# Optimization experiments

Hardware: AMD Instinct MI355X
Metric: run time of the kernel (lower is better)

The kernel has to match this reference:

```python
import math
import jax, jax.numpy as jnp
import numpy as np

N, S, D = 1024, 256, 256
C, R, CLASSES = 256, 64, 1000


def setup_inputs() -> dict:
    key = jax.random.key(0)
    ks = jax.random.split(key, 10)
    inv_sqrt_d = 1.0 / math.sqrt(D)
    return {
        "q": jax.random.normal(ks[0], (N, D), dtype=jnp.float32),
        "K": jax.random.normal(ks[1], (N, S, D), dtype=jnp.float32),
        "V": jax.random.normal(ks[2], (N, S, D), dtype=jnp.float32),
        "codebook": jax.random.normal(ks[3], (C, D), dtype=jnp.float32) * inv_sqrt_d,
        "residual_codebook": jax.random.normal(ks[4], (R, D), dtype=jnp.float32) * inv_sqrt_d,
        "Wq": jax.random.normal(ks[5], (D, D), dtype=jnp.float32) * inv_sqrt_d,
        "residual_logit": jnp.zeros((), dtype=jnp.float32),
        "Wc": jax.random.normal(ks[6], (CLASSES, D), dtype=jnp.float32) * inv_sqrt_d,
        "bc": jnp.zeros((CLASSES,), dtype=jnp.float32),
        "Wr": jax.random.normal(ks[7], (D, D), dtype=jnp.float32) * inv_sqrt_d,
        "br": jnp.zeros((D,), dtype=jnp.float32),
    }


def reference(q, K, V, codebook, residual_codebook, Wq, residual_logit, Wc, bc, Wr, br):
    scale = math.sqrt(q.shape[-1])
    q_proj = q @ Wq.T  # [N,D]

    # --- base codebook pass ---
    code_weights = jax.nn.softmax(jnp.einsum('nd,cd->nc', q_proj, codebook) / scale, axis=-1)
    slot_code_weights = jax.nn.softmax(jnp.einsum('nsd,cd->nsc', K, codebook) / scale, axis=-1)
    slot_code_summaries = jnp.einsum('nsc,nsd->ncd', slot_code_weights, V)
    base_summary = jnp.einsum('nc,ncd->nd', code_weights, slot_code_summaries)
    base_weights = jnp.einsum('nc,nsc->ns', code_weights, slot_code_weights)

    # --- residual quantization pass ---
    query_residual = q_proj - code_weights @ codebook
    slot_residual = K - jnp.einsum('nsc,cd->nsd', slot_code_weights, codebook)
    residual_code_weights = jax.nn.softmax(
        jnp.einsum('nd,rd->nr', query_residual, residual_codebook) / scale, axis=-1)
    residual_slot_code_weights = jax.nn.softmax(
        jnp.einsum('nsd,rd->nsr', slot_residual, residual_codebook) / scale, axis=-1)
    residual_slot_summaries = jnp.einsum('nsr,nsd->nrd', residual_slot_code_weights, V)
    residual_summary = jnp.einsum('nr,nrd->nd', residual_code_weights, residual_slot_summaries)
    residual_weights = jnp.einsum('nr,nsr->ns', residual_code_weights, residual_slot_code_weights)

    gate = jax.nn.sigmoid(residual_logit)
    summary = base_summary + gate * residual_summary
    effective_weights = (base_weights + gate * residual_weights) / (1.0 + gate)

    logits = summary @ Wc.T + bc
    recon = summary @ Wr.T + br
    return (logits, recon, effective_weights)
```

## Files before the change

### kernel.cpp

```cpp
#include <hip/hip_runtime.h>
#include <hip/hip_bf16.h>
#include <math.h>

#define N_   1024
#define S_   256
#define D_   256
#define C_   256
#define R_   64
#define CLS_ 1000
#define INV16 0.0625f

typedef unsigned short ushortT;
typedef unsigned int uint32;
typedef short bf8 __attribute__((ext_vector_type(8)));
typedef float f4 __attribute__((ext_vector_type(4)));

static __device__ __forceinline__ float bf2f(uint32 u){
  return __uint_as_float(u << 16);
}
static __device__ __forceinline__ ushortT f2bf(float f){
  uint32 x = __float_as_uint(f);
  uint32 r = x + 0x7FFFu + ((x >> 16) & 1u);
  return (ushortT)(r >> 16);
}
static __device__ __forceinline__ uint32 packbf(float a, float b){
  return ((uint32)f2bf(b) << 16) | (uint32)f2bf(a);
}
static __device__ __forceinline__ float wred_max(float v){
  for (int o = 32; o; o >>= 1) v = fmaxf(v, __shfl_xor(v, o));
  return v;
}
static __device__ __forceinline__ float wred_sum(float v){
  for (int o = 32; o; o >>= 1) v += __shfl_xor(v, o);
  return v;
}
static __device__ __forceinline__ int swz(int row, int colbyte){
  return row*512 + ((colbyte & ~15) ^ ((row & 7) << 4)) + (colbyte & 15);
}
static __device__ __forceinline__ int pkidx(int row, int col, int nfrag){
  int ks = col >> 5, hi = (col >> 3) & 3, e = col & 7;
  int frag = row >> 4, l15p = row & 15;
  return ((ks*nfrag + frag)*64 + hi*16 + l15p)*8 + e;
}

__global__ __launch_bounds__(256) void k0(const float* __restrict__ cb,
    const float* __restrict__ rcb, const float* __restrict__ Wc,
    const float* __restrict__ Wr, ushortT* __restrict__ a1pk,
    ushortT* __restrict__ Wcr_bf, float* __restrict__ MT_f32,
    ushortT* __restrict__ mtpk)
{
  __shared__ float rl[D_];
  int bid = blockIdx.x, t = threadIdx.x;
  int gtid = bid*256 + t;
  int stride = gridDim.x*256;
  for (int e = gtid; e < (C_ + R_)*D_; e += stride){
    int row = e >> 8, col = e & 255;
    float v = (row < C_) ? cb[e] : rcb[e - C_*D_];
    a1pk[pkidx(row, col, 20)] = f2bf(v);
  }
  for (int e = gtid; e < CLS_*D_; e += stride) Wcr_bf[e] = f2bf(Wc[e]);
  for (int e = gtid; e < D_*D_; e += stride)  Wcr_bf[CLS_*D_ + e] = f2bf(Wr[e]);
  for (int e = gtid; e < 24*D_; e += stride)  Wcr_bf[1256*D_ + e] = 0;

  if (bid < R_){
    rl[t] = rcb[bid*D_ + t];
    __syncthreads();
    float acc = 0.f;
    const float* crow = cb + t*D_;
    #pragma unroll 8
    for (int k = 0; k < D_; k += 4){
      float4 w = *(const float4*)(crow + k);
      acc += w.x*rl[k] + w.y*rl[k+1] + w.z*rl[k+2] + w.w*rl[k+3];
    }
    MT_f32[bid*C_ + t] = acc;
    mtpk[pkidx(bid, t, 4)] = f2bf(acc);
  }
}

#define G4 4
__global__ __launch_bounds__(256) void k1(const float* __restrict__ q,
    const float* __restrict__ cb, const float* __restrict__ rcb,
    const float* __restrict__ Wq, const float* __restrict__ MT_f32,
    float* __restrict__ cw_ws, float* __restrict__ rcw_ws)
{
  __shared__ float qv[G4][D_], qp[G4][D_], cwl[G4][C_];
  __shared__ float redA[G4][4], redB2[G4][4];
  int n0 = blockIdx.x*G4, t = threadIdx.x;
  #pragma unroll
  for (int g = 0; g < G4; g++) qv[g][t] = q[(n0+g)*D_ + t];
  __syncthreads();
  {
    float acc[G4] = {0.f,0.f,0.f,0.f};
    const float* wrow = Wq + t*D_;
    #pragma unroll 4
    for (int k = 0; k < D_; k += 4){
      float4 w = *(const float4*)(wrow + k);
      #pragma unroll
      for (int g = 0; g < G4; g++)
        acc[g] += qv[g][k]*w.x + qv[g][k+1]*w.y + qv[g][k+2]*w.z + qv[g][k+3]*w.w;
    }
    #pragma unroll
    for (int g = 0; g < G4; g++) qp[g][t] = acc[g];
  }
  __syncthreads();
  float L[G4] = {0.f,0.f,0.f,0.f};
  {
    const float* crow = cb + t*D_;
    #pragma unroll 4
    for (int k = 0; k < D_; k += 4){
      float4 w = *(const float4*)(crow + k);
      #pragma unroll
      for (int g = 0; g < G4; g++)
        L[g] += qp[g][k]*w.x + qp[g][k+1]*w.y + qp[g][k+2]*w.z + qp[g][k+3]*w.w;
    }
  }
  float m[G4], e[G4], s[G4];
  #pragma unroll
  for (int g = 0; g < G4; g++){ L[g] *= INV16; m[g] = wred_max(L[g]); }
  if ((t & 63) == 0)
    #pragma unroll
    for (int g = 0; g < G4; g++) redA[g][t >> 6] = m[g];
  __syncthreads();
  #pragma unroll
  for (int g = 0; g < G4; g++){
    m[g] = fmaxf(fmaxf(redA[g][0], redA[g][1]), fmaxf(redA[g][2], redA[g][3]));
    e[g] = __expf(L[g] - m[g]);
    s[g] = wred_sum(e[g]);
  }
  if ((t & 63) == 0)
    #pragma unroll
    for (int g = 0; g < G4; g++) redB2[g][t >> 6] = s[g];
  __syncthreads();
  #pragma unroll
  for (int g = 0; g < G4; g++){
    float ss = redB2[g][0] + redB2[g][1] + redB2[g][2] + redB2[g][3];
    float w = e[g] / ss;
    cwl[g][t] = w;
    cw_ws[(n0+g)*C_ + t] = w;
  }
  __syncthreads();
  if (t < R_){
    float qd[G4] = {0.f,0.f,0.f,0.f}, md[G4] = {0.f,0.f,0.f,0.f};
    const float* rrow = rcb + t*D_;
    const float* mrow = MT_f32 + t*C_;
    #pragma unroll 4
    for (int k = 0; k < D_; k += 4){
      float4 wv = *(const float4*)(rrow + k);
      float4 mv = *(const float4*)(mrow + k);
      #pragma unroll
      for (int g = 0; g < G4; g++){
        qd[g] += qp[g][k]*wv.x + qp[g][k+1]*wv.y + qp[g][k+2]*wv.z + qp[g][k+3]*wv.w;
        md[g] += cwl[g][k]*mv.x + cwl[g][k+1]*mv.y + cwl[g][k+2]*mv.z + cwl[g][k+3]*mv.w;
      }
    }
    #pragma unroll
    for (int g = 0; g < G4; g++){
      float Lr = (qd[g] - md[g]) * INV16;
      float mr = wred_max(Lr);
      float er = __expf(Lr - mr);
      float sr = wred_sum(er);
      rcw_ws[(n0+g)*R_ + t] = er / sr;
    }
  }
}

__global__ __launch_bounds__(256) void k2a(const float* __restrict__ Kt,
    const ushortT* __restrict__ a1pk, const ushortT* __restrict__ mtpk,
    const float* __restrict__ cw_ws, const float* __restrict__ rcw_ws,
    const float* __restrict__ rlogit, float* __restrict__ comb_ws,
    float* __restrict__ out_ew)
{
  __shared__ __align__(16) ushortT Ktile[64*256];
  __shared__ __align__(16) ushortT Wtile[64*256];
  __shared__ float redS[4][64], redW[4][64];

  int bx  = blockIdx.x;
  int n   = bx >> 2;
  int s0  = (bx & 3) * 64;
  int tid = threadIdx.x;
  int lane = tid & 63, w = tid >> 6;
  int l15 = lane & 15, l4 = lane >> 4;
  float gate  = 1.f / (1.f + __expf(-rlogit[0]));
  float inv1g = 1.f / (1.f + gate);

  const float* Kn = Kt + (size_t)n*S_*D_ + (size_t)s0*D_;

  #pragma unroll
  for (int j = 0; j < 8; j++){
    int ch = tid + j*256;
    int row = ch >> 5, blk = ch & 31;
    const float* src = Kn + row*D_ + blk*8;
    float4 a = *(const float4*)src;
    float4 b = *(const float4*)(src + 4);
    uint4 wv = {packbf(a.x,a.y), packbf(a.z,a.w), packbf(b.x,b.y), packbf(b.z,b.w)};
    *(uint4*)((char*)Ktile + swz(row, blk*16)) = wv;
  }
  __syncthreads();

  const ushortT* a1b = a1pk + (size_t)lane*8;
  bf8 bnxC[4], bnxR[4];
  #pragma unroll
  for (int f = 0; f < 4; f++){
    bnxC[f] = *(const bf8*)(a1b + (size_t)((w + 4*f)*64)*8);
    bnxR[f] = *(const bf8*)(a1b + (size_t)((16 + f)*64)*8);
  }
  f4 accC[4][4]; f4 accR[4];
  #pragma unroll
  for (int f = 0; f < 4; f++){
    accR[f] = (f4)0.f;
    #pragma unroll
    for (int sj = 0; sj < 4; sj++) accC[f][sj] = (f4)0.f;
  }
  #pragma unroll
  for (int ks = 0; ks < 8; ks++){
    bf8 kf0 = *(const bf8*)((const char*)Ktile + swz(     l15, ks*64 + l4*16));
    bf8 kf1 = *(const bf8*)((const char*)Ktile + swz(16 + l15, ks*64 + l4*16));
    bf8 kf2 = *(const bf8*)((const char*)Ktile + swz(32 + l15, ks*64 + l4*16));
    bf8 kf3 = *(const bf8*)((const char*)Ktile + swz(48 + l15, ks*64 + l4*16));
    bf8 kfw = *(const bf8*)((const char*)Ktile + swz(w*16 + l15, ks*64 + l4*16));
    #pragma unroll
    for (int f = 0; f < 4; f++){
      bf8 aC = bnxC[f], aR = bnxR[f];
      if (ks < 7){
        bnxC[f] = *(const bf8*)(a1b + (size_t)(((ks+1)*20 + w + 4*f)*64)*8);
        bnxR[f] = *(const bf8*)(a1b + (size_t)(((ks+1)*20 + 16 + f)*64)*8);
      }
      accC[f][0] = __builtin_amdgcn_mfma_f32_16x16x32_bf16(aC, kf0, accC[f][0], 0, 0, 0);
      accC[f][1] = __builtin_amdgcn_mfma_f32_16x16x32_bf16(aC, kf1, accC[f][1], 0, 0, 0);
      accC[f][2] = __builtin_amdgcn_mfma_f32_16x16x32_bf16(aC, kf2, accC[f][2], 0, 0, 0);
      accC[f][3] = __builtin_amdgcn_mfma_f32_16x16x32_bf16(aC, kf3, accC[f][3], 0, 0, 0);
      accR[f]    = __builtin_amdgcn_mfma_f32_16x16x32_bf16(aR, kfw, accR[f],    0, 0, 0);
    }
  }

  float4 cwv[4];
  #pragma unroll
  for (int f = 0; f < 4; f++)
    cwv[f] = *(const float4*)(cw_ws + n*C_ + (w + 4*f)*16 + l4*4);
  float se[4] = {0,0,0,0}, sb[4] = {0,0,0,0};
  #pragma unroll
  for (int f = 0; f < 4; f++){
    int cbyte = ((w + 4*f)*16 + l4*4) * 2;
    #pragma unroll
    for (int sj = 0; sj < 4; sj++){
      float e0 = __expf(accC[f][sj][0] * INV16);
      float e1 = __expf(accC[f][sj][1] * INV16);
      float e2 = __expf(accC[f][sj][2] * INV16);
      float e3 = __expf(accC[f][sj][3] * INV16);
      se[sj] += (e0 + e1) + (e2 + e3);
      sb[sj] += e0*cwv[f].x + e1*cwv[f].y + e2*cwv[f].z + e3*cwv[f].w;
      int s_ = sj*16 + l15;
      *(uint32*)((char*)Wtile + swz(s_, cbyte))     = packbf(e0, e1);
      *(uint32*)((char*)Wtile + swz(s_, cbyte + 4)) = packbf(e2, e3);
    }
  }
  #pragma unroll
  for (int sj = 0; sj < 4; sj++){
    se[sj] += __shfl_xor(se[sj], 16); se[sj] += __shfl_xor(se[sj], 32);
    sb[sj] += __shfl_xor(sb[sj], 16); sb[sj] += __shfl_xor(sb[sj], 32);
  }
  if (l4 == 0){
    #pragma unroll
    for (int sj = 0; sj < 4; sj++){
      redS[w][sj*16 + l15] = se[sj];
      redW[w][sj*16 + l15] = sb[sj];
    }
  }
  __syncthreads();

  float bw_q, rcp_q;
  {
    int sq = w*16 + l15;
    float sS = redS[0][sq] + redS[1][sq] + redS[2][sq] + redS[3][sq];
    float sW = redW[0][sq] + redW[1][sq] + redW[2][sq] + redW[3][sq];
    bw_q  = sW / sS;
    rcp_q = 1.f / sS;
  }

  const ushortT* mtb = mtpk + (size_t)lane*8;
  bf8 mnx[4];
  #pragma unroll
  for (int fr = 0; fr < 4; fr++)
    mnx[fr] = *(const bf8*)(mtb + (size_t)(fr*64)*8);
  f4 wm[4];
  #pragma unroll
  for (int fr = 0; fr < 4; fr++) wm[fr] = (f4)0.f;
  #pragma unroll
  for (int ks = 0; ks < 8; ks++){
    bf8 wb = *(const bf8*)((const char*)Wtile + swz(w*16 + l15, ks*64 + l4*16));
    #pragma unroll
    for (int fr = 0; fr < 4; fr++){
      bf8 a = mnx[fr];
      if (ks < 7) mnx[fr] = *(const bf8*)(mtb + (size_t)(((ks+1)*4 + fr)*64)*8);
      wm[fr] = __builtin_amdgcn_mfma_f32_16x16x32_bf16(a, wb, wm[fr], 0, 0, 0);
    }
  }

  float4 rcwv = *(const float4*)(rcw_ws + n*R_ + 0);
  float se3 = 0.f, sc3 = 0.f;
  #pragma unroll
  for (int fr = 0; fr < 4; fr++){
    float4 rv = *(const float4*)(rcw_ws + n*R_ + fr*16 + l4*4);
    float e0 = __expf((accR[fr][0] - wm[fr][0]*rcp_q) * INV16);
    float e1 = __expf((accR[fr][1] - wm[fr][1]*rcp_q) * INV16);
    float e2 = __expf((accR[fr][2] - wm[fr][2]*rcp_q) * INV16);
    float e3 = __expf((accR[fr][3] - wm[fr][3]*rcp_q) * INV16);
    se3 += (e0 + e1) + (e2 + e3);
    sc3 += e0*rv.x + e1*rv.y + e2*rv.z + e3*rv.w;
  }
  (void)rcwv;
  se3 += __shfl_xor(se3, 16); se3 += __shfl_xor(se3, 32);
  sc3 += __shfl_xor(sc3, 16); sc3 += __shfl_xor(sc3, 32);
  float comb = bw_q + gate * (sc3 / se3);
  if (l4 == 0){
    int sabs = n*S_ + s0 + w*16 + l15;
    out_ew[sabs]  = comb * inv1g;
    comb_ws[sabs] = comb;
  }
}

__global__ __launch_bounds__(256) void k2b(const float* __restrict__ Vt,
    const float* __restrict__ comb_ws, float* __restrict__ sum_ws)
{
  __shared__ float cl[S_];
  __shared__ float4 part[4][64];
  int n = blockIdx.x, tid = threadIdx.x;
  int lane = tid & 63, w = tid >> 6;
  cl[tid] = comb_ws[n*S_ + tid];
  __syncthreads();
  const float* Vn = Vt + (size_t)n*S_*D_ + (size_t)(w*64)*D_ + lane*4;
  float4 a0 = {0,0,0,0}, a1 = {0,0,0,0};
  #pragma unroll 8
  for (int j = 0; j < 64; j += 2){
    float4 v0 = *(const float4*)(Vn + (size_t)j*D_);
    float4 v1 = *(const float4*)(Vn + (size_t)(j+1)*D_);
    float c0 = cl[w*64 + j], c1 = cl[w*64 + j + 1];
    a0.x = fmaf(c0, v0.x, a0.x); a0.y = fmaf(c0, v0.y, a0.y);
    a0.z = fmaf(c0, v0.z, a0.z); a0.w = fmaf(c0, v0.w, a0.w);
    a1.x = fmaf(c1, v1.x, a1.x); a1.y = fmaf(c1, v1.y, a1.y);
    a1.z = fmaf(c1, v1.z, a1.z); a1.w = fmaf(c1, v1.w, a1.w);
  }
  float4 acc = {a0.x+a1.x, a0.y+a1.y, a0.z+a1.z, a0.w+a1.w};
  part[w][lane] = acc;
  __syncthreads();
  if (tid < 64){
    float4 p0 = part[0][tid], p1 = part[1][tid], p2 = part[2][tid], p3 = part[3][tid];
    float4 r = {p0.x+p1.x+p2.x+p3.x, p0.y+p1.y+p2.y+p3.y,
                p0.z+p1.z+p2.z+p3.z, p0.w+p1.w+p2.w+p3.w};
    *(float4*)(sum_ws + (size_t)n*D_ + tid*4) = r;
  }
}

__global__ __launch_bounds__(256) void k3(const float* __restrict__ sum_ws,
    const ushortT* __restrict__ Wcr_bf, const float* __restrict__ bc,
    const float* __restrict__ br, float* __restrict__ out)
{
  __shared__ __align__(16) ushortT Stile[64*256];
  int bx = blockIdx.x;
  int ot = bx >> 4;
  int nt = bx & 15;
  int tid = threadIdx.x;
  int lane = tid & 63, wid = tid >> 6;
  int l15 = lane & 15, l4 = lane >> 4;

  const float* Sp = sum_ws + (size_t)nt*64*D_;
  #pragma unroll
  for (int j = 0; j < 8; j++){
    int ch = tid + j*256;
    int row = ch >> 5, blk = ch & 31;
    const float* src = Sp + row*D_ + blk*8;
    float4 a = *(const float4*)src;
    float4 b = *(const float4*)(src + 4);
    uint4 wv = {packbf(a.x,a.y), packbf(a.z,a.w), packbf(b.x,b.y), packbf(b.z,b.w)};
    *(uint4*)((char*)Stile + swz(row, blk*16)) = wv;
  }
  __syncthreads();

  int o0 = ot*64 + wid*16;
  const ushortT* Ap = Wcr_bf + (size_t)(o0 + l15)*D_ + l4*8;
  f4 acc[4];
  #pragma unroll
  for (int j = 0; j < 4; j++) acc[j] = (f4)0.f;
  #pragma unroll
  for (int k = 0; k < 8; k++){
    bf8 a = *(const bf8*)(Ap + k*32);
    #pragma unroll
    for (int nj = 0; nj < 4; nj++){
      bf8 b = *(const bf8*)((const char*)Stile + swz(nj*16 + l15, k*64 + l4*16));
      acc[nj] = __builtin_amdgcn_mfma_f32_16x16x32_bf16(a, b, acc[nj], 0, 0, 0);
    }
  }
  int obase = o0 + l4*4;
  if (obase < 1256){
    float4 bias;
    if (obase < CLS_) bias = *(const float4*)(bc + obase);
    else              bias = *(const float4*)(br + (obase - CLS_));
    #pragma unroll
    for (int nj = 0; nj < 4; nj++){
      int nn = nt*64 + nj*16 + l15;
      float4 v = {acc[nj][0]+bias.x, acc[nj][1]+bias.y, acc[nj][2]+bias.z, acc[nj][3]+bias.w};
      if (obase < CLS_) *(float4*)(out + (size_t)nn*CLS_ + obase) = v;
      else              *(float4*)(out + (size_t)N_*CLS_ + (size_t)nn*D_ + (obase - CLS_)) = v;
    }
  }
}

extern "C" void kernel_launch(void* const* d_in, const int* in_sizes, int n_in,
                              void* d_out, int out_size, void* d_ws, size_t ws_size,
                              hipStream_t stream)
{
  const float* q    = (const float*)d_in[0];
  const float* Kt   = (const float*)d_in[1];
  const float* Vt   = (const float*)d_in[2];
  const float* cb   = (const float*)d_in[3];
  const float* rcb  = (const float*)d_in[4];
  const float* Wq   = (const float*)d_in[5];
  const float* rlg  = (const float*)d_in[6];
  const float* Wc   = (const float*)d_in[7];
  const float* bc   = (const float*)d_in[8];
  const float* Wr   = (const float*)d_in[9];
  const float* br   = (const float*)d_in[10];
  float* out = (float*)d_out;
  float* ws  = (float*)d_ws;

  float* cw_ws   = ws;
  float* rcw_ws  = ws + 262144;
  float* sum_ws  = ws + 327680;
  float* comb_ws = ws + 589824;
  float* MT_f32  = ws + 851968;
  ushortT* a1pk   = (ushortT*)(ws + 868352);
  ushortT* mtpk   = a1pk + (C_ + R_)*D_;
  ushortT* Wcr_bf = mtpk + R_*C_;

  float* out_logits = out;
  float* out_ew     = out + (size_t)N_*CLS_ + (size_t)N_*D_;

  k0 <<<128,   256, 0, stream>>>(cb, rcb, Wc, Wr, a1pk, Wcr_bf, MT_f32, mtpk);
  k1 <<<N_/G4, 256, 0, stream>>>(q, cb, rcb, Wq, MT_f32, cw_ws, rcw_ws);
  k2a<<<N_*4,  256, 0, stream>>>(Kt, a1pk, mtpk, cw_ws, rcw_ws, rlg, comb_ws, out_ew);
  k2b<<<N_,    256, 0, stream>>>(Vt, comb_ws, sum_ws);
  k3 <<<320,   256, 0, stream>>>(sum_ws, Wcr_bf, bc, br, out_logits);
}
```

Baseline: 232.0 us.

## Halve k2a slot tile to 32 and split residual work across warp pairs

The k2a kernel now handles 32 slots per block instead of 64 and launches twice as many blocks, with a launch-bounds hint asking for four blocks per CU. The residual-codebook MFMAs are split so warp pairs share R fragments across the two 16-slot groups, and an extra shared-memory reduction combines their partial softmax sums. The aim is lower register and LDS use per block for higher occupancy, and better latency hiding on the memory-bound K stream. In exchange, the shared codebook fragments are reloaded by twice as many blocks, and each block pays an additional barrier.

```diff
diff --git a/kernel.cpp b/kernel.cpp
--- a/kernel.cpp
+++ b/kernel.cpp
@@ -164,29 +164,32 @@
   }
 }
 
-__global__ __launch_bounds__(256) void k2a(const float* __restrict__ Kt,
+__global__ __launch_bounds__(256, 4) void k2a(const float* __restrict__ Kt,
     const ushortT* __restrict__ a1pk, const ushortT* __restrict__ mtpk,
     const float* __restrict__ cw_ws, const float* __restrict__ rcw_ws,
     const float* __restrict__ rlogit, float* __restrict__ comb_ws,
     float* __restrict__ out_ew)
 {
-  __shared__ __align__(16) ushortT Ktile[64*256];
-  __shared__ __align__(16) ushortT Wtile[64*256];
-  __shared__ float redS[4][64], redW[4][64];
+  __shared__ __align__(16) ushortT Ktile[32*256];
+  __shared__ __align__(16) ushortT Wtile[32*256];
+  __shared__ float redS[4][32], redW[4][32];
+  __shared__ float red3S[4][32], red3W[4][32];
 
   int bx  = blockIdx.x;
-  int n   = bx >> 2;
-  int s0  = (bx & 3) * 64;
+  int n   = bx >> 3;
+  int s0  = (bx & 7) * 32;
   int tid = threadIdx.x;
   int lane = tid & 63, w = tid >> 6;
   int l15 = lane & 15, l4 = lane >> 4;
+  int rp  = w >> 1;
+  int sjr = w & 1;
   float gate  = 1.f / (1.f + __expf(-rlogit[0]));
   float inv1g = 1.f / (1.f + gate);
 
   const float* Kn = Kt + (size_t)n*S_*D_ + (size_t)s0*D_;
 
   #pragma unroll
-  for (int j = 0; j < 8; j++){
+  for (int j = 0; j < 4; j++){
     int ch = tid + j*256;
     int row = ch >> 5, blk = ch & 31;
     const float* src = Kn + row*D_ + blk*8;
@@ -198,51 +201,55 @@
   __syncthreads();
 
   const ushortT* a1b = a1pk + (size_t)lane*8;
-  bf8 bnxC[4], bnxR[4];
-  #pragma unroll
-  for (int f = 0; f < 4; f++){
+  bf8 bnxC[4], bnxR[2];
+  #pragma unroll
+  for (int f = 0; f < 4; f++)
     bnxC[f] = *(const bf8*)(a1b + (size_t)((w + 4*f)*64)*8);
-    bnxR[f] = *(const bf8*)(a1b + (size_t)((16 + f)*64)*8);
-  }
-  f4 accC[4][4]; f4 accR[4];
-  #pragma unroll
-  for (int f = 0; f < 4; f++){
-    accR[f] = (f4)0.f;
-    #pragma unroll
-    for (int sj = 0; sj < 4; sj++) accC[f][sj] = (f4)0.f;
-  }
+  #pragma unroll
+  for (int i = 0; i < 2; i++)
+    bnxR[i] = *(const bf8*)(a1b + (size_t)((16 + 2*rp + i)*64)*8);
+  f4 accC[4][2]; f4 accR[2];
+  accR[0] = (f4)0.f; accR[1] = (f4)0.f;
+  #pragma unroll
+  for (int f = 0; f < 4; f++){ accC[f][0] = (f4)0.f; accC[f][1] = (f4)0.f; }
   #pragma unroll
   for (int ks = 0; ks < 8; ks++){
     bf8 kf0 = *(const bf8*)((const char*)Ktile + swz(     l15, ks*64 + l4*16));
     bf8 kf1 = *(const bf8*)((const char*)Ktile + swz(16 + l15, ks*64 + l4*16));
-    bf8 kf2 = *(const bf8*)((const char*)Ktile + swz(32 + l15, ks*64 + l4*16));
-    bf8 kf3 = *(const bf8*)((const char*)Ktile + swz(48 + l15, ks*64 + l4*16));
-    bf8 kfw = *(const bf8*)((const char*)Ktile + swz(w*16 + l15, ks*64 + l4*16));
+    bf8 kfr = sjr ? kf1 : kf0;
     #pragma unroll
     for (int f = 0; f < 4; f++){
-      bf8 aC = bnxC[f], aR = bnxR[f];
-      if (ks < 7){
+      bf8 aC = bnxC[f];
+      if (ks < 7)
         bnxC[f] = *(const bf8*)(a1b + (size_t)(((ks+1)*20 + w + 4*f)*64)*8);
-        bnxR[f] = *(const bf8*)(a1b + (size_t)(((ks+1)*20 + 16 + f)*64)*8);
-      }
       accC[f][0] = __builtin_amdgcn_mfma_f32_16x16x32_bf16(aC, kf0, accC[f][0], 0, 0, 0);
       accC[f][1] = __builtin_amdgcn_mfma_f32_16x16x32_bf16(aC, kf1, accC[f][1], 0, 0, 0);
-      accC[f][2] = __builtin_amdgcn_mfma_f32_16x16x32_bf16(aC, kf2, accC[f][2], 0, 0, 0);
-      accC[f][3] = __builtin_amdgcn_mfma_f32_16x16x32_bf16(aC, kf3, accC[f][3], 0, 0, 0);
-      accR[f]    = __builtin_amdgcn_mfma_f32_16x16x32_bf16(aR, kfw, accR[f],    0, 0, 0);
-    }
-  }
+    }
+    #pragma unroll
+    for (int i = 0; i < 2; i++){
+      bf8 aR = bnxR[i];
+      if (ks < 7)
+        bnxR[i] = *(const bf8*)(a1b + (size_t)(((ks+1)*20 + 16 + 2*rp + i)*64)*8);
+      accR[i] = __builtin_amdgcn_mfma_f32_16x16x32_bf16(aR, kfr, accR[i], 0, 0, 0);
+    }
+  }
+
+  const ushortT* mtb = mtpk + (size_t)lane*8;
+  bf8 mnx[2];
+  #pragma unroll
+  for (int i = 0; i < 2; i++)
+    mnx[i] = *(const bf8*)(mtb + (size_t)((2*rp + i)*64)*8);
 
   float4 cwv[4];
   #pragma unroll
   for (int f = 0; f < 4; f++)
     cwv[f] = *(const float4*)(cw_ws + n*C_ + (w + 4*f)*16 + l4*4);
-  float se[4] = {0,0,0,0}, sb[4] = {0,0,0,0};
+  float se[2] = {0,0}, sb[2] = {0,0};
   #pragma unroll
   for (int f = 0; f < 4; f++){
     int cbyte = ((w + 4*f)*16 + l4*4) * 2;
     #pragma unroll
-    for (int sj = 0; sj < 4; sj++){
+    for (int sj = 0; sj < 2; sj++){
       float e0 = __expf(accC[f][sj][0] * INV16);
       float e1 = __expf(accC[f][sj][1] * INV16);
       float e2 = __expf(accC[f][sj][2] * INV16);
@@ -255,13 +262,13 @@
     }
   }
   #pragma unroll
-  for (int sj = 0; sj < 4; sj++){
+  for (int sj = 0; sj < 2; sj++){
     se[sj] += __shfl_xor(se[sj], 16); se[sj] += __shfl_xor(se[sj], 32);
     sb[sj] += __shfl_xor(sb[sj], 16); sb[sj] += __shfl_xor(sb[sj], 32);
   }
   if (l4 == 0){
     #pragma unroll
-    for (int sj = 0; sj < 4; sj++){
+    for (int sj = 0; sj < 2; sj++){
       redS[w][sj*16 + l15] = se[sj];
       redW[w][sj*16 + l15] = sb[sj];
     }
@@ -270,52 +277,55 @@
 
   float bw_q, rcp_q;
   {
-    int sq = w*16 + l15;
+    int sq = sjr*16 + l15;
     float sS = redS[0][sq] + redS[1][sq] + redS[2][sq] + redS[3][sq];
     float sW = redW[0][sq] + redW[1][sq] + redW[2][sq] + redW[3][sq];
-    bw_q  = sW / sS;
     rcp_q = 1.f / sS;
-  }
-
-  const ushortT* mtb = mtpk + (size_t)lane*8;
-  bf8 mnx[4];
-  #pragma unroll
-  for (int fr = 0; fr < 4; fr++)
-    mnx[fr] = *(const bf8*)(mtb + (size_t)(fr*64)*8);
-  f4 wm[4];
-  #pragma unroll
-  for (int fr = 0; fr < 4; fr++) wm[fr] = (f4)0.f;
+    bw_q  = sW * rcp_q;
+  }
+
+  f4 wm[2]; wm[0] = (f4)0.f; wm[1] = (f4)0.f;
   #pragma unroll
   for (int ks = 0; ks < 8; ks++){
-    bf8 wb = *(const bf8*)((const char*)Wtile + swz(w*16 + l15, ks*64 + l4*16));
-    #pragma unroll
-    for (int fr = 0; fr < 4; fr++){
-      bf8 a = mnx[fr];
-      if (ks < 7) mnx[fr] = *(const bf8*)(mtb + (size_t)(((ks+1)*4 + fr)*64)*8);
-      wm[fr] = __builtin_amdgcn_mfma_f32_16x16x32_bf16(a, wb, wm[fr], 0, 0, 0);
-    }
-  }
-
-  float4 rcwv = *(const float4*)(rcw_ws + n*R_ + 0);
+    bf8 wb = *(const bf8*)((const char*)Wtile + swz(sjr*16 + l15, ks*64 + l4*16));
+    #pragma unroll
+    for (int i = 0; i < 2; i++){
+      bf8 a = mnx[i];
+      if (ks < 7)
+        mnx[i] = *(const bf8*)(mtb + (size_t)(((ks+1)*4 + 2*rp + i)*64)*8);
+      wm[i] = __builtin_amdgcn_mfma_f32_16x16x32_bf16(a, wb, wm[i], 0, 0, 0);
+    }
+  }
+
   float se3 = 0.f, sc3 = 0.f;
   #pragma unroll
-  for (int fr = 0; fr < 4; fr++){
-    float4 rv = *(const float4*)(rcw_ws + n*R_ + fr*16 + l4*4);
-    float e0 = __expf((accR[fr][0] - wm[fr][0]*rcp_q) * INV16);
-    float e1 = __expf((accR[fr][1] - wm[fr][1]*rcp_q) * INV16);
-    float e2 = __expf((accR[fr][2] - wm[fr][2]*rcp_q) * INV16);
-    float e3 = __expf((accR[fr][3] - wm[fr][3]*rcp_q) * INV16);
+  for (int i = 0; i < 2; i++){
+    float4 rv = *(const float4*)(rcw_ws + n*R_ + (2*rp + i)*16 + l4*4);
+    float e0 = __expf((accR[i][0] - wm[i][0]*rcp_q) * INV16);
+    float e1 = __expf((accR[i][1] - wm[i][1]*rcp_q) * INV16);
+    float e2 = __expf((accR[i][2] - wm[i][2]*rcp_q) * INV16);
+    float e3 = __expf((accR[i][3] - wm[i][3]*rcp_q) * INV16);
     se3 += (e0 + e1) + (e2 + e3);
     sc3 += e0*rv.x + e1*rv.y + e2*rv.z + e3*rv.w;
   }
-  (void)rcwv;
   se3 += __shfl_xor(se3, 16); se3 += __shfl_xor(se3, 32);
   sc3 += __shfl_xor(sc3, 16); sc3 += __shfl_xor(sc3, 32);
-  float comb = bw_q + gate * (sc3 / se3);
   if (l4 == 0){
-    int sabs = n*S_ + s0 + w*16 + l15;
-    out_ew[sabs]  = comb * inv1g;
-    comb_ws[sabs] = comb;
+    red3S[w][sjr*16 + l15] = se3;
+    red3W[w][sjr*16 + l15] = sc3;
+  }
+  __syncthreads();
+
+  if (w < 2){
+    int sq = w*16 + l15;
+    float sS3 = red3S[w][sq] + red3S[w + 2][sq];
+    float sW3 = red3W[w][sq] + red3W[w + 2][sq];
+    float comb = bw_q + gate * (sW3 / sS3);
+    if (l4 == 0){
+      int sabs = n*S_ + s0 + sq;
+      out_ew[sabs]  = comb * inv1g;
+      comb_ws[sabs] = comb;
+    }
   }
 }
 
@@ -437,7 +447,7 @@
 
   k0 <<<128,   256, 0, stream>>>(cb, rcb, Wc, Wr, a1pk, Wcr_bf, MT_f32, mtpk);
   k1 <<<N_/G4, 256, 0, stream>>>(q, cb, rcb, Wq, MT_f32, cw_ws, rcw_ws);
-  k2a<<<N_*4,  256, 0, stream>>>(Kt, a1pk, mtpk, cw_ws, rcw_ws, rlg, comb_ws, out_ew);
+  k2a<<<N_*8,  256, 0, stream>>>(Kt, a1pk, mtpk, cw_ws, rcw_ws, rlg, comb_ws, out_ew);
   k2b<<<N_,    256, 0, stream>>>(Vt, comb_ws, sum_ws);
   k3 <<<320,   256, 0, stream>>>(sum_ws, Wcr_bf, bc, br, out_logits);
 }
```

After: 224.6 us. -3.2%, faster.
